# Kernel tuning notes

Measured on AMD Instinct MI355X. Metric: run time of the kernel, lower is better.

The kernel has to match this reference:

```python
import jax, jax.numpy as jnp
import numpy as np

DS_DIM = 2
N_EXPERTS = 64
N_CLASSES = 26
IMG = 68
BATCH = 8192
FLAT = 1960  # 10 * 14 * 14 after two conv+pool stages


def _conv2d(x, w, b):
    # x: [B, Cin, H, W], w: [Cout, Cin, kh, kw]
    y = jax.lax.conv_general_dilated(
        x, w, window_strides=(1, 1), padding='VALID',
        dimension_numbers=('NCHW', 'OIHW', 'NCHW'))
    return y + b[None, :, None, None]


def _maxpool2(x):
    return jax.lax.reduce_window(
        x, -jnp.inf, jax.lax.max,
        window_dimensions=(1, 1, 2, 2), window_strides=(1, 1, 2, 2),
        padding='VALID')


def setup_inputs() -> dict:
    key = jax.random.key(0)
    ks = jax.random.split(key, 14)
    x = jax.random.normal(ks[0], (BATCH, DS_DIM), dtype=jnp.float32)
    cls_idx = jax.random.randint(ks[1], (BATCH,), 0, N_CLASSES)
    images = jax.random.normal(ks[2], (N_CLASSES, 1, IMG, IMG), dtype=jnp.float32)
    s = 0.05
    conv1_w = jax.random.normal(ks[3], (5, 1, 5, 5), dtype=jnp.float32) * s
    conv1_b = jax.random.normal(ks[4], (5,), dtype=jnp.float32) * s
    conv2_w = jax.random.normal(ks[5], (10, 5, 5, 5), dtype=jnp.float32) * s
    conv2_b = jax.random.normal(ks[6], (10,), dtype=jnp.float32) * s
    fc1_w = jax.random.normal(ks[7], (500, FLAT + DS_DIM), dtype=jnp.float32) * s
    fc1_b = jax.random.normal(ks[8], (500,), dtype=jnp.float32) * s
    fc2_w = jax.random.normal(ks[9], (N_EXPERTS, 500), dtype=jnp.float32) * s
    fc2_b = jax.random.normal(ks[10], (N_EXPERTS,), dtype=jnp.float32) * s
    # geotorch-constrained expert matrices: B_A positive-semidefinite, C_A skew
    raw_b = jax.random.normal(ks[11], (N_EXPERTS, DS_DIM, DS_DIM), dtype=jnp.float32)
    A_B = jnp.einsum('nik,njk->nij', raw_b, raw_b) * 0.1        # PSD
    raw_c = jax.random.normal(ks[12], (N_EXPERTS, DS_DIM, DS_DIM), dtype=jnp.float32)
    A_C = (raw_c - jnp.swapaxes(raw_c, -1, -2)) * 0.5            # skew
    x_tar = jax.random.normal(ks[13], (1, DS_DIM), dtype=jnp.float32)
    return {'x': x, 'cls_idx': cls_idx, 'images': images,
            'conv1_w': conv1_w, 'conv1_b': conv1_b,
            'conv2_w': conv2_w, 'conv2_b': conv2_b,
            'fc1_w': fc1_w, 'fc1_b': fc1_b,
            'fc2_w': fc2_w, 'fc2_b': fc2_b,
            'A_B': A_B, 'A_C': A_C, 'x_tar': x_tar}


def reference(x, cls_idx, images, conv1_w, conv1_b, conv2_w, conv2_b,
              fc1_w, fc1_b, fc2_w, fc2_b, A_B, A_C, x_tar):
    # gating CNN: gather per-sample image by class index
    img = images[cls_idx]                             # [B, 1, 68, 68]
    h = _maxpool2(jax.nn.relu(_conv2d(img, conv1_w, conv1_b)))   # [B, 5, 32, 32]
    h = _maxpool2(jax.nn.relu(_conv2d(h, conv2_w, conv2_b)))     # [B, 10, 14, 14]
    h = h.reshape(h.shape[0], -1)                     # [B, 1960]
    h = jnp.concatenate([h, x], axis=1)               # [B, 1962]
    h = jax.nn.relu(h @ fc1_w.T + fc1_b)              # [B, 500]
    w_all = jax.nn.softmax(h @ fc2_w.T + fc2_b, axis=1)  # [B, N]
    # fused expert weighted-sum (original: python loop over N tiny matmuls)
    A = A_B + A_C                                     # [N, d, d]
    diff = x_tar - x                                  # [B, d]
    s_all = jnp.einsum('bn,nij,bj->bi', w_all, A, diff)
    return s_all
```

## Files before the change

kernel.cpp:

```cpp
#include <hip/hip_runtime.h>

#define WS_FEAT   0
#define WS_FC1P   51136
#define WS_FC2T   64160
#define WS_AFLAT  96160
#define WS_WX     96416

__global__ __launch_bounds__(256) void k_cnn(
    const float* __restrict__ images,
    const float* __restrict__ c1w, const float* __restrict__ c1b,
    const float* __restrict__ c2w, const float* __restrict__ c2b,
    const float* __restrict__ fc2w, const float* __restrict__ fc1w,
    const float* __restrict__ A_B, const float* __restrict__ A_C,
    float* __restrict__ ws)
{
    const int bid = blockIdx.x;
    const int t = threadIdx.x;

    if (bid >= 104) {
        if (bid == 104) {
            float* fc2T = ws + WS_FC2T;
            for (int i = t; i < 32000; i += 256) {
                int e = i / 500, j = i - e * 500;
                fc2T[j * 64 + e] = fc2w[i];
            }
        } else {
            float* Af = ws + WS_AFLAT;
            if (t < 256) Af[t] = A_B[t] + A_C[t];
            float* Wx = ws + WS_WX;
            for (int i = t; i < 1000; i += 256) {
                int j = i >> 1, k = i & 1;
                Wx[i] = fc1w[j * 1962 + 1960 + k];
            }
        }
        return;
    }

    const int c  = bid >> 2, q = bid & 3;
    const int qy = q >> 1,  qx = q & 1;

    __shared__ float simg[1600];
    __shared__ float sc1[5 * 324];
    __shared__ float sw1[125];
    __shared__ float sb1[5];
    __shared__ float sw2[1250];
    __shared__ float sb2[10];

    {
        const float* ib = images + c * (68 * 68) + (28 * qy) * 68 + 28 * qx;
        for (int i = t; i < 800; i += 256) {
            int r = i / 20, c2 = i - r * 20;
            *(float2*)&simg[r * 40 + c2 * 2] = *(const float2*)&ib[r * 68 + c2 * 2];
        }
    }
    for (int i = t; i < 125; i += 256)  sw1[i] = c1w[i];
    if (t < 5)  sb1[t] = c1b[t];
    for (int i = t; i < 1250; i += 256) sw2[i] = c2w[i];
    if (t < 10) sb2[t] = c2b[t];
    __syncthreads();

    float b1r[5];
#pragma unroll
    for (int o = 0; o < 5; ++o) b1r[o] = sb1[o];

    for (int idx = t; idx < 324; idx += 256) {
        int ry = idx / 18, rx = idx - ry * 18;
        float ir[6][6];
#pragma unroll
        for (int a = 0; a < 6; ++a)
#pragma unroll
            for (int b2 = 0; b2 < 3; ++b2) {
                float2 v = *(const float2*)&simg[(2 * ry + a) * 40 + 2 * rx + 2 * b2];
                ir[a][2 * b2] = v.x; ir[a][2 * b2 + 1] = v.y;
            }
#pragma unroll
        for (int oc = 0; oc < 5; ++oc) {
            float a00 = b1r[oc], a01 = b1r[oc], a10 = b1r[oc], a11 = b1r[oc];
#pragma unroll
            for (int ky = 0; ky < 5; ++ky)
#pragma unroll
                for (int kx = 0; kx < 5; ++kx) {
                    float w = sw1[oc * 25 + ky * 5 + kx];
                    a00 += w * ir[ky][kx];
                    a01 += w * ir[ky][kx + 1];
                    a10 += w * ir[ky + 1][kx];
                    a11 += w * ir[ky + 1][kx + 1];
                }
            float v = fmaxf(fmaxf(fmaxf(a00, a01), fmaxf(a10, a11)), 0.f);
            sc1[oc * 324 + idx] = v;
        }
    }
    __syncthreads();

    for (int idx = t; idx < 490; idx += 256) {
        int oc = idx / 49, pos = idx - oc * 49;
        int py = pos / 7,  px = pos - py * 7;
        float a00 = sb2[oc], a01 = a00, a10 = a00, a11 = a00;
#pragma unroll
        for (int ic = 0; ic < 5; ++ic) {
            float ir[6][6];
#pragma unroll
            for (int a = 0; a < 6; ++a)
#pragma unroll
                for (int b2 = 0; b2 < 3; ++b2) {
                    float2 v = *(const float2*)&sc1[ic * 324 + (2 * py + a) * 18 + 2 * px + 2 * b2];
                    ir[a][2 * b2] = v.x; ir[a][2 * b2 + 1] = v.y;
                }
#pragma unroll
            for (int ky = 0; ky < 5; ++ky)
#pragma unroll
                for (int kx = 0; kx < 5; ++kx) {
                    float w = sw2[oc * 125 + ic * 25 + ky * 5 + kx];
                    a00 += w * ir[ky][kx];
                    a01 += w * ir[ky][kx + 1];
                    a10 += w * ir[ky + 1][kx];
                    a11 += w * ir[ky + 1][kx + 1];
                }
        }
        float v = fmaxf(fmaxf(fmaxf(a00, a01), fmaxf(a10, a11)), 0.f);
        int gpy = qy * 7 + py, gpx = qx * 7 + px;
        ws[WS_FEAT + c * 1960 + oc * 196 + gpy * 14 + gpx] = v;
    }
}

__global__ __launch_bounds__(256) void k_fc1(
    const float* __restrict__ fc1w, const float* __restrict__ fc1b,
    float* __restrict__ ws)
{
    const int lane = threadIdx.x & 63;
    const int w    = threadIdx.x >> 6;
    const int j    = blockIdx.x * 4 + w;

    float wreg[31];
#pragma unroll
    for (int i = 0; i < 31; ++i) {
        int k = lane + 64 * i;
        wreg[i] = (k < 1960) ? fc1w[j * 1962 + k] : 0.f;
    }
    const float bj = fc1b[j];
    const float* feat = ws + WS_FEAT;
    float* fc1p = ws + WS_FC1P;

    for (int c = 0; c < 26; ++c) {
        const float* f = feat + c * 1960;
        float acc = 0.f;
#pragma unroll
        for (int i = 0; i < 31; ++i) acc += wreg[i] * f[lane + 64 * i];
#pragma unroll
        for (int off = 32; off >= 1; off >>= 1) acc += __shfl_xor(acc, off);
        if (lane == 0) fc1p[c * 500 + j] = acc + bj;
    }
}

__global__ __launch_bounds__(256) void k_moe(
    const float* __restrict__ x, const int* __restrict__ cls,
    const float* __restrict__ fc2b, const float* __restrict__ x_tar,
    const float* __restrict__ ws, float* __restrict__ out)
{
    __shared__ float sh[8][500];
    __shared__ float sred[2048];
    const int t = threadIdx.x;
    const int b0 = blockIdx.x * 8;
    const float* fc1p = ws + WS_FC1P;
    const float* fc2T = ws + WS_FC2T;
    const float* Af   = ws + WS_AFLAT;
    const float* Wx   = ws + WS_WX;

    int cs[8]; float xs0[8], xs1[8];
#pragma unroll
    for (int s = 0; s < 8; ++s) {
        cs[s]  = cls[b0 + s];
        xs0[s] = x[2 * (b0 + s)];
        xs1[s] = x[2 * (b0 + s) + 1];
    }
    for (int j = t; j < 500; j += 256) {
        float2 wx = *(const float2*)&Wx[2 * j];
#pragma unroll
        for (int s = 0; s < 8; ++s) {
            float v = fc1p[cs[s] * 500 + j] + xs0[s] * wx.x + xs1[s] * wx.y;
            sh[s][j] = fmaxf(v, 0.f);
        }
    }
    __syncthreads();

    const int e = t & 63, p = t >> 6;
    float acc[8];
#pragma unroll
    for (int s = 0; s < 8; ++s) acc[s] = 0.f;

    const int jbeg = p * 128;
    const int jend = (p == 3) ? 500 : (jbeg + 128);
    for (int j4 = jbeg; j4 < jend; j4 += 4) {
        float w0 = fc2T[(j4 + 0) * 64 + e];
        float w1 = fc2T[(j4 + 1) * 64 + e];
        float w2 = fc2T[(j4 + 2) * 64 + e];
        float w3 = fc2T[(j4 + 3) * 64 + e];
#pragma unroll
        for (int s = 0; s < 8; ++s) {
            float4 h4 = *(const float4*)&sh[s][j4];
            acc[s] += h4.x * w0 + h4.y * w1 + h4.z * w2 + h4.w * w3;
        }
    }
#pragma unroll
    for (int s = 0; s < 8; ++s) sred[p * 512 + s * 64 + e] = acc[s];
    __syncthreads();

    const float xt0 = x_tar[0], xt1 = x_tar[1];
    const float be = fc2b[e];
    const float4 a4 = *(const float4*)&Af[4 * e];
#pragma unroll
    for (int half = 0; half < 2; ++half) {
        int s = half * 4 + p;
        float logit = be + sred[s * 64 + e] + sred[512 + s * 64 + e]
                    + sred[1024 + s * 64 + e] + sred[1536 + s * 64 + e];
        float m = logit;
#pragma unroll
        for (int off = 32; off >= 1; off >>= 1) m = fmaxf(m, __shfl_xor(m, off));
        float ex = __expf(logit - m);
        float sum = ex;
        float m0 = ex * a4.x, m1 = ex * a4.y, m2 = ex * a4.z, m3 = ex * a4.w;
#pragma unroll
        for (int off = 32; off >= 1; off >>= 1) {
            sum += __shfl_xor(sum, off);
            m0 += __shfl_xor(m0, off);
            m1 += __shfl_xor(m1, off);
            m2 += __shfl_xor(m2, off);
            m3 += __shfl_xor(m3, off);
        }
        if (e == 0) {
            int b = b0 + s;
            float d0 = xt0 - x[2 * b], d1 = xt1 - x[2 * b + 1];
            float inv = 1.f / sum;
            out[2 * b]     = (m0 * d0 + m1 * d1) * inv;
            out[2 * b + 1] = (m2 * d0 + m3 * d1) * inv;
        }
    }
}

extern "C" void kernel_launch(void* const* d_in, const int* in_sizes, int n_in,
                              void* d_out, int out_size, void* d_ws, size_t ws_size,
                              hipStream_t stream) {
    const float* x      = (const float*)d_in[0];
    const int*   cls    = (const int*)  d_in[1];
    const float* images = (const float*)d_in[2];
    const float* c1w    = (const float*)d_in[3];
    const float* c1b    = (const float*)d_in[4];
    const float* c2w    = (const float*)d_in[5];
    const float* c2b    = (const float*)d_in[6];
    const float* fc1w   = (const float*)d_in[7];
    const float* fc1b   = (const float*)d_in[8];
    const float* fc2w   = (const float*)d_in[9];
    const float* fc2b   = (const float*)d_in[10];
    const float* A_B    = (const float*)d_in[11];
    const float* A_C    = (const float*)d_in[12];
    const float* x_tar  = (const float*)d_in[13];
    float* out = (float*)d_out;
    float* ws  = (float*)d_ws;

    k_cnn<<<106, 256, 0, stream>>>(images, c1w, c1b, c2w, c2b, fc2w, fc1w, A_B, A_C, ws);
    k_fc1<<<125, 256, 0, stream>>>(fc1w, fc1b, ws);
    k_moe<<<1024, 256, 0, stream>>>(x, cls, fc2b, x_tar, ws, out);
}
```

Measured before the change: 148.8 us.

## Split CNN into separate conv kernels, split-K fc1 with atomics, pack fc2 weights

The fused 106-block CNN kernel becomes two kernels. A 522-block conv1 kernel computes one output channel per block, and a 260-block conv2 kernel reads conv1 results through a global workspace. fc1 is split into two K halves across 250 blocks, which combine with atomicAdd into a buffer zeroed by an auxiliary block. fc2 weights are pre-packed as float4 per expert so the moe kernel does vector loads. The goal is more parallelism in the small front stages; the cost is an extra kernel launch, global round-trips for conv1 activations, and atomics.

```diff
diff --git a/kernel.cpp b/kernel.cpp
--- a/kernel.cpp
+++ b/kernel.cpp
@@ -1,28 +1,30 @@
 #include <hip/hip_runtime.h>
 
-#define WS_FEAT   0
-#define WS_FC1P   51136
-#define WS_FC2T   64160
-#define WS_AFLAT  96160
-#define WS_WX     96416
-
-__global__ __launch_bounds__(256) void k_cnn(
-    const float* __restrict__ images,
-    const float* __restrict__ c1w, const float* __restrict__ c1b,
-    const float* __restrict__ c2w, const float* __restrict__ c2b,
-    const float* __restrict__ fc2w, const float* __restrict__ fc1w,
-    const float* __restrict__ A_B, const float* __restrict__ A_C,
-    float* __restrict__ ws)
-{
-    const int bid = blockIdx.x;
-    const int t = threadIdx.x;
-
-    if (bid >= 104) {
-        if (bid == 104) {
-            float* fc2T = ws + WS_FC2T;
-            for (int i = t; i < 32000; i += 256) {
-                int e = i / 500, j = i - e * 500;
-                fc2T[j * 64 + e] = fc2w[i];
+#define WS_SC1    0
+#define WS_FEAT   133120
+#define WS_FC1P   184080
+#define WS_FC2P   197080
+#define WS_AFLAT  229080
+#define WS_WX     229336
+
+__global__ __launch_bounds__(256) void k_conv1(
+    const float* __restrict__ images, const float* __restrict__ c1w,
+    const float* __restrict__ c1b, const float* __restrict__ fc2w,
+    const float* __restrict__ fc1w, const float* __restrict__ A_B,
+    const float* __restrict__ A_C, float* __restrict__ ws)
+{
+    const int b = blockIdx.x, t = threadIdx.x;
+    if (b >= 520) {
+        if (b == 520) {
+            float* P = ws + WS_FC2P;
+            for (int i = t; i < 8000; i += 256) {
+                int j4 = i >> 6, e = i & 63;
+                float4 v;
+                v.x = fc2w[e * 500 + 4 * j4 + 0];
+                v.y = fc2w[e * 500 + 4 * j4 + 1];
+                v.z = fc2w[e * 500 + 4 * j4 + 2];
+                v.w = fc2w[e * 500 + 4 * j4 + 3];
+                *(float4*)&P[i * 4] = v;
             }
         } else {
             float* Af = ws + WS_AFLAT;
@@ -32,123 +34,117 @@
                 int j = i >> 1, k = i & 1;
                 Wx[i] = fc1w[j * 1962 + 1960 + k];
             }
+            float* fp = ws + WS_FC1P;
+            for (int i = t; i < 13000; i += 256) fp[i] = 0.f;
         }
         return;
     }
 
-    const int c  = bid >> 2, q = bid & 3;
-    const int qy = q >> 1,  qx = q & 1;
-
-    __shared__ float simg[1600];
-    __shared__ float sc1[5 * 324];
-    __shared__ float sw1[125];
-    __shared__ float sb1[5];
-    __shared__ float sw2[1250];
-    __shared__ float sb2[10];
-
-    {
-        const float* ib = images + c * (68 * 68) + (28 * qy) * 68 + 28 * qx;
-        for (int i = t; i < 800; i += 256) {
-            int r = i / 20, c2 = i - r * 20;
-            *(float2*)&simg[r * 40 + c2 * 2] = *(const float2*)&ib[r * 68 + c2 * 2];
-        }
-    }
-    for (int i = t; i < 125; i += 256)  sw1[i] = c1w[i];
-    if (t < 5)  sb1[t] = c1b[t];
-    for (int i = t; i < 1250; i += 256) sw2[i] = c2w[i];
-    if (t < 10) sb2[t] = c2b[t];
+    const int c = b / 20, r = b - c * 20;
+    const int oc = r >> 2, g = r & 3;
+    const int py = g * 8 + (t >> 5), px = t & 31;
+
+    float wr[25];
+#pragma unroll
+    for (int i = 0; i < 25; ++i) wr[i] = c1w[oc * 25 + i];
+    const float bias = c1b[oc];
+
+    const float* im = images + c * 4624 + (2 * py) * 68 + 2 * px;
+    float ir[6][6];
+#pragma unroll
+    for (int a = 0; a < 6; ++a)
+#pragma unroll
+        for (int q = 0; q < 3; ++q) {
+            float2 v = *(const float2*)&im[a * 68 + 2 * q];
+            ir[a][2 * q] = v.x; ir[a][2 * q + 1] = v.y;
+        }
+
+    float a00 = bias, a01 = bias, a10 = bias, a11 = bias;
+#pragma unroll
+    for (int ky = 0; ky < 5; ++ky)
+#pragma unroll
+        for (int kx = 0; kx < 5; ++kx) {
+            float w = wr[ky * 5 + kx];
+            a00 += w * ir[ky][kx];     a01 += w * ir[ky][kx + 1];
+            a10 += w * ir[ky + 1][kx]; a11 += w * ir[ky + 1][kx + 1];
+        }
+    float v = fmaxf(fmaxf(fmaxf(a00, a01), fmaxf(a10, a11)), 0.f);
+    ws[WS_SC1 + ((c * 5 + oc) * 32 + py) * 32 + px] = v;
+}
+
+__global__ __launch_bounds__(256) void k_conv2(
+    const float* __restrict__ c2w, const float* __restrict__ c2b,
+    float* __restrict__ ws)
+{
+    const int b = blockIdx.x, t = threadIdx.x;
+    const int c = b / 10, oc = b - c * 10;
+
+    __shared__ float sw[125];
+    if (t < 125) sw[t] = c2w[oc * 125 + t];
     __syncthreads();
-
-    float b1r[5];
-#pragma unroll
-    for (int o = 0; o < 5; ++o) b1r[o] = sb1[o];
-
-    for (int idx = t; idx < 324; idx += 256) {
-        int ry = idx / 18, rx = idx - ry * 18;
+    if (t >= 196) return;
+
+    const int py = t / 14, px = t - py * 14;
+    const float bias = c2b[oc];
+    float a00 = bias, a01 = bias, a10 = bias, a11 = bias;
+
+    const float* base = ws + WS_SC1 + c * 5120 + (2 * py) * 32 + 2 * px;
+#pragma unroll
+    for (int ic = 0; ic < 5; ++ic) {
+        const float* s1 = base + ic * 1024;
         float ir[6][6];
 #pragma unroll
         for (int a = 0; a < 6; ++a)
 #pragma unroll
-            for (int b2 = 0; b2 < 3; ++b2) {
-                float2 v = *(const float2*)&simg[(2 * ry + a) * 40 + 2 * rx + 2 * b2];
-                ir[a][2 * b2] = v.x; ir[a][2 * b2 + 1] = v.y;
-            }
-#pragma unroll
-        for (int oc = 0; oc < 5; ++oc) {
-            float a00 = b1r[oc], a01 = b1r[oc], a10 = b1r[oc], a11 = b1r[oc];
-#pragma unroll
-            for (int ky = 0; ky < 5; ++ky)
-#pragma unroll
-                for (int kx = 0; kx < 5; ++kx) {
-                    float w = sw1[oc * 25 + ky * 5 + kx];
-                    a00 += w * ir[ky][kx];
-                    a01 += w * ir[ky][kx + 1];
-                    a10 += w * ir[ky + 1][kx];
-                    a11 += w * ir[ky + 1][kx + 1];
-                }
-            float v = fmaxf(fmaxf(fmaxf(a00, a01), fmaxf(a10, a11)), 0.f);
-            sc1[oc * 324 + idx] = v;
-        }
-    }
-    __syncthreads();
-
-    for (int idx = t; idx < 490; idx += 256) {
-        int oc = idx / 49, pos = idx - oc * 49;
-        int py = pos / 7,  px = pos - py * 7;
-        float a00 = sb2[oc], a01 = a00, a10 = a00, a11 = a00;
-#pragma unroll
-        for (int ic = 0; ic < 5; ++ic) {
-            float ir[6][6];
-#pragma unroll
-            for (int a = 0; a < 6; ++a)
-#pragma unroll
-                for (int b2 = 0; b2 < 3; ++b2) {
-                    float2 v = *(const float2*)&sc1[ic * 324 + (2 * py + a) * 18 + 2 * px + 2 * b2];
-                    ir[a][2 * b2] = v.x; ir[a][2 * b2 + 1] = v.y;
-                }
-#pragma unroll
-            for (int ky = 0; ky < 5; ++ky)
-#pragma unroll
-                for (int kx = 0; kx < 5; ++kx) {
-                    float w = sw2[oc * 125 + ic * 25 + ky * 5 + kx];
-                    a00 += w * ir[ky][kx];
-                    a01 += w * ir[ky][kx + 1];
-                    a10 += w * ir[ky + 1][kx];
-                    a11 += w * ir[ky + 1][kx + 1];
-                }
-        }
-        float v = fmaxf(fmaxf(fmaxf(a00, a01), fmaxf(a10, a11)), 0.f);
-        int gpy = qy * 7 + py, gpx = qx * 7 + px;
-        ws[WS_FEAT + c * 1960 + oc * 196 + gpy * 14 + gpx] = v;
-    }
+            for (int q = 0; q < 3; ++q) {
+                float2 v = *(const float2*)&s1[a * 32 + 2 * q];
+                ir[a][2 * q] = v.x; ir[a][2 * q + 1] = v.y;
+            }
+#pragma unroll
+        for (int ky = 0; ky < 5; ++ky)
+#pragma unroll
+            for (int kx = 0; kx < 5; ++kx) {
+                float w = sw[ic * 25 + ky * 5 + kx];
+                a00 += w * ir[ky][kx];     a01 += w * ir[ky][kx + 1];
+                a10 += w * ir[ky + 1][kx]; a11 += w * ir[ky + 1][kx + 1];
+            }
+    }
+    float v = fmaxf(fmaxf(fmaxf(a00, a01), fmaxf(a10, a11)), 0.f);
+    ws[WS_FEAT + c * 1960 + oc * 196 + py * 14 + px] = v;
 }
 
 __global__ __launch_bounds__(256) void k_fc1(
     const float* __restrict__ fc1w, const float* __restrict__ fc1b,
     float* __restrict__ ws)
 {
-    const int lane = threadIdx.x & 63;
-    const int w    = threadIdx.x >> 6;
-    const int j    = blockIdx.x * 4 + w;
-
-    float wreg[31];
-#pragma unroll
-    for (int i = 0; i < 31; ++i) {
-        int k = lane + 64 * i;
-        wreg[i] = (k < 1960) ? fc1w[j * 1962 + k] : 0.f;
-    }
-    const float bj = fc1b[j];
+    const int lane = threadIdx.x & 63, w = threadIdx.x >> 6;
+    const int jg = blockIdx.x >> 1, half = blockIdx.x & 1;
+    const int j = jg * 4 + w;
+    const int kbase = half * 980;
+
+    float wreg[16];
+#pragma unroll
+    for (int i = 0; i < 16; ++i) {
+        int kl = lane + 64 * i;
+        wreg[i] = (kl < 980) ? fc1w[j * 1962 + kbase + kl] : 0.f;
+    }
+    const float bj = (half == 0) ? fc1b[j] : 0.f;
     const float* feat = ws + WS_FEAT;
     float* fc1p = ws + WS_FC1P;
 
     for (int c = 0; c < 26; ++c) {
-        const float* f = feat + c * 1960;
-        float acc = 0.f;
-#pragma unroll
-        for (int i = 0; i < 31; ++i) acc += wreg[i] * f[lane + 64 * i];
+        const float* f = feat + c * 1960 + kbase;
+        float acc0 = 0.f, acc1 = 0.f;
+#pragma unroll
+        for (int i = 0; i < 16; i += 2) {
+            int k0 = lane + 64 * i, k1 = lane + 64 * (i + 1);
+            acc0 += wreg[i]     * f[(k0 < 980) ? k0 : 0];
+            acc1 += wreg[i + 1] * f[(k1 < 980) ? k1 : 0];
+        }
+        float acc = acc0 + acc1;
 #pragma unroll
         for (int off = 32; off >= 1; off >>= 1) acc += __shfl_xor(acc, off);
-        if (lane == 0) fc1p[c * 500 + j] = acc + bj;
+        if (lane == 0) atomicAdd(&fc1p[c * 500 + j], acc + bj);
     }
 }
 
@@ -162,7 +158,7 @@
     const int t = threadIdx.x;
     const int b0 = blockIdx.x * 8;
     const float* fc1p = ws + WS_FC1P;
-    const float* fc2T = ws + WS_FC2T;
+    const float* fc2P = ws + WS_FC2P;
     const float* Af   = ws + WS_AFLAT;
     const float* Wx   = ws + WS_WX;
 
@@ -188,17 +184,14 @@
 #pragma unroll
     for (int s = 0; s < 8; ++s) acc[s] = 0.f;
 
-    const int jbeg = p * 128;
-    const int jend = (p == 3) ? 500 : (jbeg + 128);
-    for (int j4 = jbeg; j4 < jend; j4 += 4) {
-        float w0 = fc2T[(j4 + 0) * 64 + e];
-        float w1 = fc2T[(j4 + 1) * 64 + e];
-        float w2 = fc2T[(j4 + 2) * 64 + e];
-        float w3 = fc2T[(j4 + 3) * 64 + e];
+    const int gbeg = p * 32;
+    const int gend = (p == 3) ? 125 : (gbeg + 32);
+    for (int j4 = gbeg; j4 < gend; ++j4) {
+        float4 wv = *(const float4*)&fc2P[(j4 * 64 + e) * 4];
 #pragma unroll
         for (int s = 0; s < 8; ++s) {
-            float4 h4 = *(const float4*)&sh[s][j4];
-            acc[s] += h4.x * w0 + h4.y * w1 + h4.z * w2 + h4.w * w3;
+            float4 h4 = *(const float4*)&sh[s][j4 * 4];
+            acc[s] += h4.x * wv.x + h4.y * wv.y + h4.z * wv.z + h4.w * wv.w;
         }
     }
 #pragma unroll
@@ -257,7 +250,8 @@
     float* out = (float*)d_out;
     float* ws  = (float*)d_ws;
 
-    k_cnn<<<106, 256, 0, stream>>>(images, c1w, c1b, c2w, c2b, fc2w, fc1w, A_B, A_C, ws);
-    k_fc1<<<125, 256, 0, stream>>>(fc1w, fc1b, ws);
-    k_moe<<<1024, 256, 0, stream>>>(x, cls, fc2b, x_tar, ws, out);
-}
+    k_conv1<<<522, 256, 0, stream>>>(images, c1w, c1b, fc2w, fc1w, A_B, A_C, ws);
+    k_conv2<<<260, 256, 0, stream>>>(c2w, c2b, ws);
+    k_fc1  <<<250, 256, 0, stream>>>(fc1w, fc1b, ws);
+    k_moe  <<<1024, 256, 0, stream>>>(x, cls, fc2b, x_tar, ws, out);
+}
```

After: 136.2 us. 1.09x faster.
